# Performance work log

Hardware: AMD Instinct MI355X
Metric: run time of the kernel (lower is better)

The kernel has to match this reference:

```python
import jax, jax.numpy as jnp
import numpy as np

BETA = 0.01
EPS = 1e-6

def conv3x3(x, w, b):
    y = jax.lax.conv_general_dilated(x, w, (1, 1), 'SAME',
                                     dimension_numbers=('NCHW', 'OIHW', 'NCHW'))
    return y + b[None, :, None, None]

def variance_depth_flow(gt, patch, max_depth):
    B, C, H, W = gt.shape
    py, px = H // patch, W // patch
    # [B,C,py,px,P,P]
    p = gt.reshape(B, C, py, patch, px, patch).transpose(0, 1, 2, 4, 3, 5)
    p = jnp.where((p > 0.1) & (p < max_depth), p, jnp.zeros_like(p))
    bn = jnp.log(p[..., 0, :] + EPS)   # north border  [B,C,py,px,P]
    bs = jnp.log(p[..., -1, :] + EPS)  # south
    bw = jnp.log(p[..., :, 0] + EPS)   # west
    be = jnp.log(p[..., :, -1] + EPS)  # east
    def sx(b):  # shift patches left along x (axis=3), zero-pad last column
        return jnp.concatenate([b[:, :, :, 1:], jnp.zeros_like(b[:, :, :, :1])], axis=3)
    def sy(b):  # shift patches up along y (axis=2), zero-pad last row
        return jnp.concatenate([b[:, :, 1:], jnp.zeros_like(b[:, :, :1])], axis=2)
    diffs = [be - sx(bw), bs - sy(bn), be - sx(be), bs - sy(bs), bw - sx(bw),
             bn - sy(bn), bs - sx(bs), be - sy(be), bn - sx(bn), bw - sy(bw)]
    d = jnp.stack([x.sum(-1) for x in diffs], axis=-1)  # [B,C,py,px,10]
    d = d[:, 0].transpose(0, 3, 1, 2) / patch            # [B,10,py,px]
    return d

def smooth_l1(pred, target, beta):
    d = pred - target
    ad = jnp.abs(d)
    return jnp.where(ad < beta, 0.5 * d * d / beta, ad - 0.5 * beta)

def setup_inputs() -> dict:
    key = jax.random.key(0)
    ks = jax.random.split(key, 7)
    B, FC, DC, hw, HW = 32, 256, 64, 64, 512
    feat = jax.random.normal(ks[0], (B, FC, hw, hw), dtype=jnp.float32)
    depth = jax.random.normal(ks[1], (B, DC, hw, hw), dtype=jnp.float32)
    gts = jax.random.uniform(ks[2], (B, 1, HW, HW), dtype=jnp.float32)
    W_att = jax.random.normal(ks[3], (DC, FC, 3, 3), dtype=jnp.float32) * 0.02
    b_att = jnp.zeros((DC,), dtype=jnp.float32)
    W_post = jax.random.normal(ks[4], (10, DC, 3, 3), dtype=jnp.float32) * 0.05
    b_post = jnp.zeros((10,), dtype=jnp.float32)
    return {"feat": feat, "depth": depth, "gts": gts,
            "W_att": W_att, "b_att": b_att, "W_post": W_post, "b_post": b_post}

def reference(feat, depth, gts, W_att, b_att, W_post, b_post):
    max_depth = 80.0
    n, c, h, w = depth.shape
    patch = gts.shape[2] // h
    flow_gradient = variance_depth_flow(gts, patch, max_depth)  # [B,10,h,w]
    att = jax.nn.sigmoid(conv3x3(feat, W_att, b_att))           # [B,DC,h,w]
    ds = conv3x3(att * depth, W_post, b_post)                   # [B,10,h,w]
    diff = smooth_l1(ds, flow_gradient, BETA)
    return diff.sum() / (h * w * ds.shape[0] * ds.shape[1])
```

## Files before the change

### kernel.cpp

```cpp
#include <hip/hip_runtime.h>
#include <hip/hip_bf16.h>


typedef __attribute__((ext_vector_type(4))) float f32x4;
typedef __attribute__((ext_vector_type(8))) short s16x8;

#define DEVFN __device__ __forceinline__

DEVFN float bf2f(unsigned short u){
  unsigned int x = ((unsigned int)u) << 16;
  float f; __builtin_memcpy(&f, &x, 4); return f;
}
DEVFN unsigned short f2bf(float f){
  unsigned int x; __builtin_memcpy(&x, &f, 4);
  x += 0x7fffu + ((x >> 16) & 1u);
  return (unsigned short)(x >> 16);
}

#define ASYNC16(gp, lp) __builtin_amdgcn_global_load_lds( \
    (const __attribute__((address_space(1))) unsigned int*)(gp), \
    (__attribute__((address_space(3))) unsigned int*)(lp), 16, 0, 0)

__global__ void k_weights(const float* __restrict__ Watt, const float* __restrict__ Wpost,
                          unsigned short* __restrict__ WT1, unsigned short* __restrict__ WT2){
  const int t = blockIdx.x * 256 + threadIdx.x;
  const int n1 = 9 * 64 * 256;
  if (t < n1){
    const int tap = t / (64 * 256);
    const int rem = t % (64 * 256);
    const int oc = rem / 256, ic = rem % 256;
    WT1[t] = f2bf(Watt[(oc * 256 + ic) * 9 + tap]);
  }
  const int n2 = 9 * 16 * 64;
  if (t < n2){
    const int tap = t / (16 * 64);
    const int rem = t % (16 * 64);
    const int od = rem / 64, ic = rem % 64;
    const float v = (od < 10) ? Wpost[(od * 64 + ic) * 9 + tap] : 0.0f;
    WT2[t] = f2bf(v);
  }
}

__global__ void k_borders(const float* __restrict__ gts, float* __restrict__ S,
                          float* __restrict__ out){
  const int bid = blockIdx.x, tid = threadIdx.x;
  if (bid == 0 && tid == 0) *out = 0.0f;
  __shared__ float slab[4096];
  const int rel = bid;
  const float* gp = gts + (size_t)rel * 4096;
#pragma unroll
  for (int it = 0; it < 4; ++it){
    const int id = it * 256 + tid;
    *(f32x4*)&slab[id * 4] = *(const f32x4*)&gp[id * 4];
  }
  __syncthreads();
  const int px = tid & 63, border = tid >> 6;
  float s = 0.0f;
#pragma unroll
  for (int i = 0; i < 8; ++i){
    float v;
    if (border == 0)      v = slab[px * 8 + i];
    else if (border == 1) v = slab[7 * 512 + px * 8 + i];
    else if (border == 2) v = slab[i * 512 + px * 8];
    else                  v = slab[i * 512 + px * 8 + 7];
    v = ((v > 0.1f) && (v < 80.0f)) ? v : 0.0f;
    s += __logf(v + 1e-6f);
  }
  S[((size_t)rel * 64 + px) * 4 + border] = s;
}

__global__ __launch_bounds__(512, 2) void k_gemm1(
    const float* __restrict__ feat,
    const unsigned short* __restrict__ WT1,
    const float* __restrict__ batt,
    const float* __restrict__ depth,
    unsigned short* __restrict__ adT)
{
  __shared__ unsigned short As[2][640 * 32];
  __shared__ unsigned short Bs[2][576 * 32];
  const int t = threadIdx.x;
  const int l = t & 63, w = t >> 6;
  const int b = blockIdx.x >> 3, ytile = blockIdx.x & 7;
  const int y0 = ytile * 8;
  const int fr = l & 15, g = l >> 4;
  const int x = t & 63, seg = t >> 6;
  const int sx = (x >> 1) & 3;

  f32x4 acc[4][4];
#pragma unroll
  for (int i = 0; i < 4; ++i)
#pragma unroll
    for (int j = 0; j < 4; ++j)
#pragma unroll
      for (int q = 0; q < 4; ++q) acc[i][j][q] = 0.0f;

  auto loadA = [&](int c, float* r, int j0, int j1){
#pragma unroll
    for (int j = 0; j < 5; ++j){
      if (j < j0 || j >= j1) continue;
      const int idx = seg + j * 8;
      const int yy = idx >> 2;
      const int icg = idx & 3;
      const int yr = y0 - 1 + yy;
      if (yr >= 0 && yr < 64){
        const float* gp = feat + ((size_t)(b * 256 + c * 32 + icg * 8)) * 4096
                               + (size_t)yr * 64 + x;
#pragma unroll
        for (int e = 0; e < 8; ++e) r[j * 8 + e] = gp[(size_t)e * 4096];
      } else {
#pragma unroll
        for (int e = 0; e < 8; ++e) r[j * 8 + e] = 0.0f;
      }
    }
  };
  auto writeA = [&](int d, const float* r, int j0, int j1){
#pragma unroll
    for (int j = 0; j < 5; ++j){
      if (j < j0 || j >= j1) continue;
      const int idx = seg + j * 8;
      const int yy = idx >> 2, icg = idx & 3;
      s16x8 v;
#pragma unroll
      for (int e = 0; e < 8; ++e) v[e] = (short)f2bf(r[j * 8 + e]);
      *(s16x8*)&As[d][(yy * 64 + x) * 32 + ((icg ^ sx) * 8)] = v;
    }
  };
  auto stageB = [&](int c, int d){
#pragma unroll
    for (int it = 0; it < 5; ++it){
      const int idx = it * 512 + t;
      if (idx < 2304){
        ASYNC16(WT1 + (size_t)(idx >> 2) * 256 + c * 32 + (idx & 3) * 8,
                &Bs[d][(idx >> 2) * 32 + (idx & 3) * 8]);
      }
    }
  };
  auto compute = [&](int cur, int t0, int t1){
    for (int tap = t0; tap < t1; ++tap){
      const int dy = tap / 3 - 1, dx = tap % 3 - 1;
      const int st = ((fr + dx) & 7) >> 1;
      const int grp = (g ^ st) * 8;
      s16x8 af[4], bfr[4];
#pragma unroll
      for (int i = 0; i < 4; ++i){
        const int xv = i * 16 + fr + dx;
        const bool valid = (xv >= 0) && (xv < 64);
        const int row = (w + dy + 1) * 64 + (valid ? xv : 0);
        s16x8 v = *(const s16x8*)&As[cur][row * 32 + grp];
        s16x8 z = {0,0,0,0,0,0,0,0};
        af[i] = valid ? v : z;
      }
#pragma unroll
      for (int j = 0; j < 4; ++j)
        bfr[j] = *(const s16x8*)&Bs[cur][(tap * 64 + j * 16 + fr) * 32 + g * 8];
#pragma unroll
      for (int i = 0; i < 4; ++i)
#pragma unroll
        for (int j = 0; j < 4; ++j)
          acc[i][j] = __builtin_amdgcn_mfma_f32_16x16x32_bf16(af[i], bfr[j], acc[i][j], 0, 0, 0);
    }
  };

  float r0[40];
  stageB(0, 0);
  loadA(0, r0, 0, 5);
  writeA(0, r0, 0, 5);
  __syncthreads();

  float r1[40];
  for (int c = 0; c < 8; ++c){
    const int cur = c & 1;
    if (c < 7){
      stageB(c + 1, cur ^ 1);
      loadA(c + 1, r1, 0, 5);
    }
    compute(cur, 0, 6);
    if (c < 7) writeA(cur ^ 1, r1, 0, 3);
    compute(cur, 6, 9);
    if (c < 7) writeA(cur ^ 1, r1, 3, 5);
    __syncthreads();
  }

  const int y = y0 + w;
#pragma unroll
  for (int j = 0; j < 4; ++j){
    const int oc = j * 16 + fr;
    const float bb = batt[oc];
    const float* dpt = depth + ((size_t)(b * 64 + oc)) * 4096 + (size_t)y * 64;
    unsigned short* op = adT + ((size_t)(b * 4096 + y * 64)) * 64 + oc;
#pragma unroll
    for (int i = 0; i < 4; ++i){
#pragma unroll
      for (int q = 0; q < 4; ++q){
        const int xo = i * 16 + g * 4 + q;
        const float v = acc[i][j][q] + bb;
        const float att = 1.0f / (1.0f + __expf(-v));
        op[(size_t)xo * 64] = f2bf(att * dpt[xo]);
      }
    }
  }
}

DEVFN float sel4(f32x4 v, int i){
  const float ab = (i & 1) ? v[1] : v[0];
  const float cd = (i & 1) ? v[3] : v[2];
  return (i & 2) ? cd : ab;
}

__global__ __launch_bounds__(512, 2) void k_gemm2(
    const unsigned short* __restrict__ adT,
    const unsigned short* __restrict__ WT2,
    const float* __restrict__ bpost,
    const f32x4* __restrict__ S,
    float* __restrict__ out)
{
  __shared__ unsigned short As[2][20480];
  __shared__ unsigned short Bs[9216];
  __shared__ float ps[8];
  const int t = threadIdx.x;
  const int l = t & 63, w = t >> 6;
  const int b = blockIdx.x >> 3, ytile = blockIdx.x & 7;
  const int y0 = ytile * 8;
  const int fr = l & 15, g = l >> 4;

  f32x4 acc[4];
#pragma unroll
  for (int i = 0; i < 4; ++i)
#pragma unroll
    for (int q = 0; q < 4; ++q) acc[i][q] = 0.0f;

  auto stageA = [&](int c, int d){
#pragma unroll
    for (int it2 = 0; it2 < 5; ++it2){
      const int it = it2 * 2 + (t >> 8);
      const int yy = y0 - 1 + it;
      const int xx = (t >> 2) & 63, icg = t & 3;
      unsigned short* lp = &As[d][(it * 64 + xx) * 32 + icg * 8];
      if (yy >= 0 && yy < 64){
        const unsigned short* gp = adT
            + ((size_t)(b * 4096 + yy * 64 + xx)) * 64 + c * 32 + icg * 8;
        ASYNC16(gp, lp);
      } else {
        s16x8 z = {0,0,0,0,0,0,0,0};
        *(s16x8*)lp = z;
      }
    }
  };
#pragma unroll
  for (int it = 0; it < 3; ++it){
    const int idx = it * 512 + t;
    if (idx < 1152) ASYNC16(WT2 + (size_t)idx * 8, Bs + idx * 8);
  }
  stageA(0, 0);
  __syncthreads();

  for (int c = 0; c < 2; ++c){
    if (c == 0) stageA(1, 1);
    const unsigned short* Ab = As[c];
    for (int tap = 0; tap < 9; ++tap){
      const int dy = tap / 3 - 1, dx = tap % 3 - 1;
      s16x8 af[4];
#pragma unroll
      for (int i = 0; i < 4; ++i){
        const int xv = i * 16 + fr + dx;
        const bool valid = (xv >= 0) && (xv < 64);
        const int wr = valid ? ((w + dy + 1) * 64 + xv) : 0;
        s16x8 v = *(const s16x8*)&Ab[wr * 32 + g * 8];
        s16x8 z = {0,0,0,0,0,0,0,0};
        af[i] = valid ? v : z;
      }
      const s16x8 bfr = *(const s16x8*)&Bs[(tap * 16 + fr) * 64 + c * 32 + g * 8];
#pragma unroll
      for (int i = 0; i < 4; ++i)
        acc[i] = __builtin_amdgcn_mfma_f32_16x16x32_bf16(af[i], bfr, acc[i], 0, 0, 0);
    }
    __syncthreads();
  }

  const unsigned aPack = (3u<<0)|(1u<<2)|(3u<<4)|(1u<<6)|(2u<<8)|(0u<<10)|(1u<<12)|(3u<<14)|(0u<<16)|(2u<<18);
  const unsigned bPack = (2u<<0)|(0u<<2)|(3u<<4)|(1u<<6)|(2u<<8)|(0u<<10)|(1u<<12)|(3u<<14)|(0u<<16)|(2u<<18);
  float lsum = 0.0f;
  const int y = y0 + w;
  if (fr < 10){
    const int od = fr;
    const int ai = (aPack >> (2 * od)) & 3;
    const int bi = (bPack >> (2 * od)) & 3;
    const bool xshift = (od & 1) == 0;
    const float bp = bpost[od];
#pragma unroll
    for (int i = 0; i < 4; ++i){
#pragma unroll
      for (int q = 0; q < 4; ++q){
        const int xo = i * 16 + g * 4 + q;
        const size_t gm = (size_t)b * 4096 + (size_t)y * 64 + xo;
        const f32x4 sa = S[gm];
        const bool nb = xshift ? (xo < 63) : (y < 63);
        const size_t ga = xshift ? (nb ? gm + 1 : gm) : (nb ? gm + 64 : gm);
        const f32x4 sbv = S[ga];
        const float sbf = nb ? sel4(sbv, bi) : 0.0f;
        const float flow = (sel4(sa, ai) - sbf) * 0.125f;
        const float dv = acc[i][q] + bp - flow;
        const float adv = fabsf(dv);
        lsum += (adv < 0.01f) ? (50.0f * dv * dv) : (adv - 0.005f);
      }
    }
  }
#pragma unroll
  for (int off = 32; off > 0; off >>= 1) lsum += __shfl_down(lsum, off);
  if (l == 0) ps[w] = lsum;
  __syncthreads();
  if (t == 0){
    float s = 0.0f;
#pragma unroll
    for (int i = 0; i < 8; ++i) s += ps[i];
    atomicAdd(out, s * (1.0f / 1310720.0f));
  }
}

extern "C" void kernel_launch(void* const* d_in, const int* in_sizes, int n_in,
                              void* d_out, int out_size, void* d_ws, size_t ws_size,
                              hipStream_t stream){
  const float* feat  = (const float*)d_in[0];
  const float* depth = (const float*)d_in[1];
  const float* gts   = (const float*)d_in[2];
  const float* Watt  = (const float*)d_in[3];
  const float* batt  = (const float*)d_in[4];
  const float* Wpost = (const float*)d_in[5];
  const float* bpost = (const float*)d_in[6];
  float* out = (float*)d_out;
  char* ws = (char*)d_ws;

  unsigned short* adT = (unsigned short*)ws;
  unsigned short* WT1 = (unsigned short*)(ws + 16777216);
  unsigned short* WT2 = (unsigned short*)(ws + 16777216 + 294912);
  float*          S   = (float*)(ws + 16777216 + 294912 + 18432);

  k_weights<<<576, 256, 0, stream>>>(Watt, Wpost, WT1, WT2);
  k_gemm1<<<256, 512, 0, stream>>>(feat, WT1, batt, depth, adT);
  k_borders<<<2048, 256, 0, stream>>>(gts, S, out);
  k_gemm2<<<256, 512, 0, stream>>>(adT, WT2, bpost, (const f32x4*)S, out);
}
```

Baseline: 93.32 us.

## Swizzle LDS tiles, pad A halo, single-buffer A with extra barrier

In the first conv GEMM, the A tile moves to a single buffer padded with zeroed halo columns (72 per row). This removes the per-lane bounds checks and selects on the shifted-tap loads. The B weight tile and both tiles of the second conv kernel get XOR-swizzled LDS placement, applied at async-load time, to cut bank conflicts. The bf16 conversion of prefetched A now overlaps compute, and the LDS write is fenced by an extra __syncthreads. That extra barrier per channel chunk trades sync cost for lower LDS use, which may allow higher occupancy.

```diff
diff --git a/kernel.cpp b/kernel.cpp
--- a/kernel.cpp
+++ b/kernel.cpp
@@ -76,7 +76,7 @@
     const float* __restrict__ depth,
     unsigned short* __restrict__ adT)
 {
-  __shared__ unsigned short As[2][640 * 32];
+  __shared__ unsigned short As[720 * 32];
   __shared__ unsigned short Bs[2][576 * 32];
   const int t = threadIdx.x;
   const int l = t & 63, w = t >> 6;
@@ -84,7 +84,6 @@
   const int y0 = ytile * 8;
   const int fr = l & 15, g = l >> 4;
   const int x = t & 63, seg = t >> 6;
-  const int sx = (x >> 1) & 3;
 
   f32x4 acc[4][4];
 #pragma unroll
@@ -94,65 +93,70 @@
 #pragma unroll
       for (int q = 0; q < 4; ++q) acc[i][j][q] = 0.0f;
 
-  auto loadA = [&](int c, float* r, int j0, int j1){
+  if (t < 80){
+    const int yy = t >> 3, k = t & 7;
+    const int xp = (k & 1) ? 65 : 0;
+    s16x8 z = {0,0,0,0,0,0,0,0};
+    *(s16x8*)&As[(yy * 72 + xp) * 32 + (k >> 1) * 8] = z;
+  }
+
+  auto stageB = [&](int c, int d){
+#pragma unroll
+    for (int it = 0; it < 5; ++it){
+      const int idx = it * 512 + t;
+      if (idx < 2304){
+        const int row = idx >> 2;
+        const int sg = (idx & 3) ^ ((row >> 1) & 3);
+        ASYNC16(WT1 + (size_t)row * 256 + c * 32 + sg * 8, &Bs[d][(size_t)idx * 8]);
+      }
+    }
+  };
+  auto loadA = [&](int c, float* rr){
 #pragma unroll
     for (int j = 0; j < 5; ++j){
-      if (j < j0 || j >= j1) continue;
       const int idx = seg + j * 8;
-      const int yy = idx >> 2;
-      const int icg = idx & 3;
+      const int yy = idx >> 2, icg = idx & 3;
       const int yr = y0 - 1 + yy;
       if (yr >= 0 && yr < 64){
         const float* gp = feat + ((size_t)(b * 256 + c * 32 + icg * 8)) * 4096
                                + (size_t)yr * 64 + x;
 #pragma unroll
-        for (int e = 0; e < 8; ++e) r[j * 8 + e] = gp[(size_t)e * 4096];
+        for (int e = 0; e < 8; ++e) rr[j * 8 + e] = gp[(size_t)e * 4096];
       } else {
 #pragma unroll
-        for (int e = 0; e < 8; ++e) r[j * 8 + e] = 0.0f;
-      }
-    }
-  };
-  auto writeA = [&](int d, const float* r, int j0, int j1){
+        for (int e = 0; e < 8; ++e) rr[j * 8 + e] = 0.0f;
+      }
+    }
+  };
+  auto cvtA = [&](const float* rr, s16x8* vA){
+#pragma unroll
+    for (int j = 0; j < 5; ++j)
+#pragma unroll
+      for (int e = 0; e < 8; ++e) vA[j][e] = (short)f2bf(rr[j * 8 + e]);
+  };
+  auto writeA = [&](const s16x8* vA){
+    const int xp = x + 1;
+    const int sx = (xp >> 1) & 3;
 #pragma unroll
     for (int j = 0; j < 5; ++j){
-      if (j < j0 || j >= j1) continue;
       const int idx = seg + j * 8;
       const int yy = idx >> 2, icg = idx & 3;
-      s16x8 v;
-#pragma unroll
-      for (int e = 0; e < 8; ++e) v[e] = (short)f2bf(r[j * 8 + e]);
-      *(s16x8*)&As[d][(yy * 64 + x) * 32 + ((icg ^ sx) * 8)] = v;
-    }
-  };
-  auto stageB = [&](int c, int d){
-#pragma unroll
-    for (int it = 0; it < 5; ++it){
-      const int idx = it * 512 + t;
-      if (idx < 2304){
-        ASYNC16(WT1 + (size_t)(idx >> 2) * 256 + c * 32 + (idx & 3) * 8,
-                &Bs[d][(idx >> 2) * 32 + (idx & 3) * 8]);
-      }
-    }
-  };
-  auto compute = [&](int cur, int t0, int t1){
+      *(s16x8*)&As[(yy * 72 + xp) * 32 + ((icg ^ sx) * 8)] = vA[j];
+    }
+  };
+  auto compute = [&](const unsigned short* Bb, int t0, int t1){
+    const int slotB = (g ^ ((fr >> 1) & 3)) * 8;
     for (int tap = t0; tap < t1; ++tap){
-      const int dy = tap / 3 - 1, dx = tap % 3 - 1;
-      const int st = ((fr + dx) & 7) >> 1;
-      const int grp = (g ^ st) * 8;
+      const int dy = tap / 3 - 1, dxp = tap % 3;
+      const int r = fr + dxp;
+      const int slotA = (g ^ ((r >> 1) & 3)) * 8;
+      const int rowb = ((w + dy + 1) * 72 + r) * 32 + slotA;
       s16x8 af[4], bfr[4];
 #pragma unroll
-      for (int i = 0; i < 4; ++i){
-        const int xv = i * 16 + fr + dx;
-        const bool valid = (xv >= 0) && (xv < 64);
-        const int row = (w + dy + 1) * 64 + (valid ? xv : 0);
-        s16x8 v = *(const s16x8*)&As[cur][row * 32 + grp];
-        s16x8 z = {0,0,0,0,0,0,0,0};
-        af[i] = valid ? v : z;
-      }
+      for (int i = 0; i < 4; ++i) af[i] = *(const s16x8*)&As[rowb + i * 512];
 #pragma unroll
       for (int j = 0; j < 4; ++j)
-        bfr[j] = *(const s16x8*)&Bs[cur][(tap * 64 + j * 16 + fr) * 32 + g * 8];
+        bfr[j] = *(const s16x8*)&Bb[(tap * 64 + j * 16 + fr) * 32 + slotB];
 #pragma unroll
       for (int i = 0; i < 4; ++i)
 #pragma unroll
@@ -161,23 +165,21 @@
     }
   };
 
-  float r0[40];
+  float rr[40]; s16x8 vA[5];
   stageB(0, 0);
-  loadA(0, r0, 0, 5);
-  writeA(0, r0, 0, 5);
+  loadA(0, rr);
+  cvtA(rr, vA);
+  writeA(vA);
   __syncthreads();
 
-  float r1[40];
   for (int c = 0; c < 8; ++c){
     const int cur = c & 1;
-    if (c < 7){
-      stageB(c + 1, cur ^ 1);
-      loadA(c + 1, r1, 0, 5);
-    }
-    compute(cur, 0, 6);
-    if (c < 7) writeA(cur ^ 1, r1, 0, 3);
-    compute(cur, 6, 9);
-    if (c < 7) writeA(cur ^ 1, r1, 3, 5);
+    if (c < 7){ stageB(c + 1, cur ^ 1); loadA(c + 1, rr); }
+    compute(Bs[cur], 0, 5);
+    if (c < 7) cvtA(rr, vA);
+    compute(Bs[cur], 5, 9);
+    __syncthreads();
+    if (c < 7) writeA(vA);
     __syncthreads();
   }
 
@@ -237,8 +239,9 @@
       const int xx = (t >> 2) & 63, icg = t & 3;
       unsigned short* lp = &As[d][(it * 64 + xx) * 32 + icg * 8];
       if (yy >= 0 && yy < 64){
+        const int sg = icg ^ ((xx >> 1) & 3);
         const unsigned short* gp = adT
-            + ((size_t)(b * 4096 + yy * 64 + xx)) * 64 + c * 32 + icg * 8;
+            + ((size_t)(b * 4096 + yy * 64 + xx)) * 64 + c * 32 + sg * 8;
         ASYNC16(gp, lp);
       } else {
         s16x8 z = {0,0,0,0,0,0,0,0};
@@ -249,7 +252,11 @@
 #pragma unroll
   for (int it = 0; it < 3; ++it){
     const int idx = it * 512 + t;
-    if (idx < 1152) ASYNC16(WT2 + (size_t)idx * 8, Bs + idx * 8);
+    if (idx < 1152){
+      const int row = idx >> 3, p = idx & 7;
+      const int sg = p ^ (row & 7);
+      ASYNC16(WT2 + (size_t)row * 64 + sg * 8, Bs + (size_t)idx * 8);
+    }
   }
   stageA(0, 0);
   __syncthreads();
@@ -257,6 +264,7 @@
   for (int c = 0; c < 2; ++c){
     if (c == 0) stageA(1, 1);
     const unsigned short* Ab = As[c];
+    const int pB = ((c * 4 + g) ^ (fr & 7)) * 8;
     for (int tap = 0; tap < 9; ++tap){
       const int dy = tap / 3 - 1, dx = tap % 3 - 1;
       s16x8 af[4];
@@ -264,12 +272,13 @@
       for (int i = 0; i < 4; ++i){
         const int xv = i * 16 + fr + dx;
         const bool valid = (xv >= 0) && (xv < 64);
-        const int wr = valid ? ((w + dy + 1) * 64 + xv) : 0;
-        s16x8 v = *(const s16x8*)&Ab[wr * 32 + g * 8];
+        const int xw = valid ? xv : 0;
+        const int slot = (g ^ ((xw >> 1) & 3)) * 8;
+        s16x8 v = *(const s16x8*)&Ab[((w + dy + 1) * 64 + xw) * 32 + slot];
         s16x8 z = {0,0,0,0,0,0,0,0};
         af[i] = valid ? v : z;
       }
-      const s16x8 bfr = *(const s16x8*)&Bs[(tap * 16 + fr) * 64 + c * 32 + g * 8];
+      const s16x8 bfr = *(const s16x8*)&Bs[(tap * 16 + fr) * 64 + pB];
 #pragma unroll
       for (int i = 0; i < 4; ++i)
         acc[i] = __builtin_amdgcn_mfma_f32_16x16x32_bf16(af[i], bfr, acc[i], 0, 0, 0);
```

Result: faster. 89.03 us (-4.6%).
